# Optimization experiments

Measured on AMD Instinct MI355X. Metric: run time of the kernel, lower is better.

## Reference

```python
import jax, jax.numpy as jnp
import numpy as np
import math

HEADS = 12
D_MODEL = 768
D_K = D_MODEL // HEADS


def setup_inputs() -> dict:
    key = jax.random.key(0)
    ks = jax.random.split(key, 11)
    B, S, D = 2, 2048, D_MODEL
    p = 0.02
    return {
        "query": jax.random.normal(ks[0], (B, S, D), jnp.float32),
        "key": jax.random.normal(ks[1], (B, S, D), jnp.float32),
        "value": jax.random.normal(ks[2], (B, S, D), jnp.float32),
        "Wq": jax.random.normal(ks[3], (D, D), jnp.float32) * p,
        "bq": jax.random.normal(ks[4], (D,), jnp.float32) * p,
        "Wk": jax.random.normal(ks[5], (D, D), jnp.float32) * p,
        "bk": jax.random.normal(ks[6], (D,), jnp.float32) * p,
        "Wv": jax.random.normal(ks[7], (D, D), jnp.float32) * p,
        "bv": jax.random.normal(ks[8], (D,), jnp.float32) * p,
        "Wo": jax.random.normal(ks[9], (D, D), jnp.float32) * p,
        "bo": jax.random.normal(ks[10], (D,), jnp.float32) * p,
    }


def reference(query, key, value, Wq, bq, Wk, bk, Wv, bv, Wo, bo):
    B, S, D = query.shape
    scale = 1.0 / math.sqrt(D_K)
    # Linear projections then split into heads: [B,S,H,Dk]
    q = (query @ Wq + bq).reshape(B, S, HEADS, D_K)
    k = (key @ Wk + bk).reshape(B, S, HEADS, D_K)
    v = (value @ Wv + bv).reshape(B, S, HEADS, D_K)
    # Full score tensor [B, i, j, H]
    scores = jnp.einsum('bihd,bjhd->bijh', q, k) * scale
    # Faithful to source: nn.Softmax(dim=1) over [b,i,j,h] -> query axis i
    attn = jax.nn.softmax(scores, axis=1)
    # dropout_prob=0 (inference/deterministic reference)
    x = jnp.einsum('bijh,bjhd->bihd', attn, v).reshape(B, S, D)
    return x @ Wo + bo
```

## Files before the change

kernel.cpp:

```cpp
#include <hip/hip_runtime.h>
#include <stdint.h>

#define HEADS 12
#define DK 64
#define DM 768
#define BT 2
#define SEQ 2048
#define ROWS (BT*SEQ)

typedef __bf16 bf16x4 __attribute__((ext_vector_type(4)));
typedef __bf16 bf16x8 __attribute__((ext_vector_type(8)));
typedef float f32x4 __attribute__((ext_vector_type(4)));

#define SCL2 0.18033688011112042f

__device__ __forceinline__ float exp2fast(float x) {
#if __has_builtin(__builtin_amdgcn_exp2f)
    return __builtin_amdgcn_exp2f(x);
#else
    return exp2f(x);
#endif
}
__device__ __forceinline__ float log2fast(float x) {
#if __has_builtin(__builtin_amdgcn_logf)
    return __builtin_amdgcn_logf(x);
#else
    return log2f(x);
#endif
}

__device__ __forceinline__ uint16_t f2bf(float f) {
    union { float f; uint32_t u; } v; v.f = f;
    uint32_t u = v.u;
    return (uint16_t)((u + 0x7FFFu + ((u >> 16) & 1u)) >> 16);
}

union U8 { uint16_t u[8]; bf16x8 v; float4 f; };

__device__ __forceinline__ bf16x8 cat44(bf16x4 lo, bf16x4 hi) {
    bf16x8 f;
    f[0] = lo[0]; f[1] = lo[1]; f[2] = lo[2]; f[3] = lo[3];
    f[4] = hi[0]; f[5] = hi[1]; f[6] = hi[2]; f[7] = hi[3];
    return f;
}

__device__ __forceinline__ bf16x8 ldfrag(const char* p) {
    bf16x4 lo = *(const bf16x4*)p;
    bf16x4 hi = *(const bf16x4*)(p + 32);
    return cat44(lo, hi);
}

typedef __attribute__((address_space(3))) void lds_vp;
typedef const __attribute__((address_space(1))) void gbl_vp;
__device__ __forceinline__ void gload16(const void* g, void* l) {
    __builtin_amdgcn_global_load_lds((gbl_vp*)g, (lds_vp*)l, 16, 0, 0);
}

__global__ __launch_bounds__(256) void k_transpose(const float* __restrict__ Wq,
                                                   const float* __restrict__ Wk,
                                                   const float* __restrict__ Wv,
                                                   const float* __restrict__ Wo,
                                                   uint16_t* __restrict__ Wqt,
                                                   uint16_t* __restrict__ Wkt,
                                                   uint16_t* __restrict__ Wvt,
                                                   uint16_t* __restrict__ Wot) {
    __shared__ float t[32][33];
    int z = blockIdx.z;
    const float* W = (z == 0) ? Wq : (z == 1) ? Wk : (z == 2) ? Wv : Wo;
    uint16_t* Wt = (z == 0) ? Wqt : (z == 1) ? Wkt : (z == 2) ? Wvt : Wot;
    int bx = blockIdx.x * 32;
    int by = blockIdx.y * 32;
    int tx = threadIdx.x & 31, ty = threadIdx.x >> 5;
#pragma unroll
    for (int r = 0; r < 32; r += 8)
        t[ty + r][tx] = W[(size_t)(bx + ty + r) * DM + by + tx];
    __syncthreads();
#pragma unroll
    for (int r = 0; r < 32; r += 8)
        Wt[(size_t)(by + ty + r) * DM + bx + tx] = f2bf(t[tx][ty + r]);
}

__global__ __launch_bounds__(256) void k_gemm_qkv(const float* __restrict__ Aq,
                                                  const float* __restrict__ Ak,
                                                  const float* __restrict__ Av,
                                                  const uint16_t* __restrict__ Wt,
                                                  const float* __restrict__ bq,
                                                  const float* __restrict__ bk,
                                                  const float* __restrict__ bv,
                                                  uint16_t* __restrict__ Qm,
                                                  uint16_t* __restrict__ Km,
                                                  uint16_t* __restrict__ VT) {
    __shared__ char smem[2 * 2 * 128 * 80];
    const int z = blockIdx.z;
    const float* A = (z == 0) ? Aq : (z == 1) ? Ak : Av;
    const uint16_t* Bt = Wt + (size_t)z * DM * DM;
    const float* bias = (z == 0) ? bq : (z == 1) ? bk : bv;
    const int tid = threadIdx.x, lane = tid & 63, w = tid >> 6;
    const int q = lane >> 4, r16 = lane & 15;
    const int mtile = blockIdx.y * 128, ntile = blockIdx.x * 128;
    const int wm = (w >> 1) * 64, wn = (w & 1) * 64;
    const int srow = tid >> 1, shalf = tid & 1;
    const float* ap = A + (size_t)(mtile + srow) * DM + shalf * 16;
    const uint16_t* bp = Bt + (size_t)(ntile + srow) * DM + shalf * 16;
    f32x4 acc[4][4] = {};
    float4 ra0 = *(const float4*)(ap + 0);
    float4 ra1 = *(const float4*)(ap + 4);
    float4 ra2 = *(const float4*)(ap + 8);
    float4 ra3 = *(const float4*)(ap + 12);
    float4 rb0 = *(const float4*)bp;
    float4 rb1 = *(const float4*)((const char*)bp + 16);
    for (int t = 0; t < 24; ++t) {
        char* As = smem + (t & 1) * 20480;
        char* Bs = As + 10240;
        U8 pk0, pk1;
        pk0.u[0] = f2bf(ra0.x); pk0.u[1] = f2bf(ra0.y); pk0.u[2] = f2bf(ra0.z); pk0.u[3] = f2bf(ra0.w);
        pk0.u[4] = f2bf(ra1.x); pk0.u[5] = f2bf(ra1.y); pk0.u[6] = f2bf(ra1.z); pk0.u[7] = f2bf(ra1.w);
        pk1.u[0] = f2bf(ra2.x); pk1.u[1] = f2bf(ra2.y); pk1.u[2] = f2bf(ra2.z); pk1.u[3] = f2bf(ra2.w);
        pk1.u[4] = f2bf(ra3.x); pk1.u[5] = f2bf(ra3.y); pk1.u[6] = f2bf(ra3.z); pk1.u[7] = f2bf(ra3.w);
        *(float4*)(As + srow * 80 + shalf * 32) = pk0.f;
        *(float4*)(As + srow * 80 + shalf * 32 + 16) = pk1.f;
        *(float4*)(Bs + srow * 80 + shalf * 32) = rb0;
        *(float4*)(Bs + srow * 80 + shalf * 32 + 16) = rb1;
        if (t < 23) {
            const float* ap2 = ap + (t + 1) * 32;
            ra0 = *(const float4*)(ap2 + 0);
            ra1 = *(const float4*)(ap2 + 4);
            ra2 = *(const float4*)(ap2 + 8);
            ra3 = *(const float4*)(ap2 + 12);
            const uint16_t* bp2 = bp + (t + 1) * 32;
            rb0 = *(const float4*)bp2;
            rb1 = *(const float4*)((const char*)bp2 + 16);
        }
        __syncthreads();
        bf16x8 af[4], bfr[4];
#pragma unroll
        for (int i = 0; i < 4; i++) {
            af[i] = ldfrag(As + (wm + i * 16 + r16) * 80 + q * 8);
            bfr[i] = ldfrag(Bs + (wn + i * 16 + r16) * 80 + q * 8);
        }
#pragma unroll
        for (int mi = 0; mi < 4; mi++)
#pragma unroll
            for (int ni = 0; ni < 4; ni++)
                acc[mi][ni] = __builtin_amdgcn_mfma_f32_16x16x32_bf16(
                    af[mi], bfr[ni], acc[mi][ni], 0, 0, 0);
    }
    if (z < 2) {
        uint16_t* out = (z == 0) ? Qm : Km;
#pragma unroll
        for (int ni = 0; ni < 4; ni++) {
            int n = ntile + wn + ni * 16 + r16;
            float bv2 = bias[n];
#pragma unroll
            for (int mi = 0; mi < 4; mi++)
#pragma unroll
                for (int r = 0; r < 4; r++) {
                    int m = mtile + wm + mi * 16 + 4 * q + r;
                    out[(size_t)m * DM + n] = f2bf(acc[mi][ni][r] + bv2);
                }
        }
    } else {
#pragma unroll
        for (int ni = 0; ni < 4; ni++) {
            int n = ntile + wn + ni * 16 + r16;
            int h = n >> 6, dk = n & 63;
            float bv2 = bias[n];
#pragma unroll
            for (int mi = 0; mi < 4; mi++) {
                int mbase = mtile + wm + mi * 16 + 4 * q;
                int b = mbase >> 11, s = mbase & 2047;
                ushort4 o;
                o.x = f2bf(acc[mi][ni][0] + bv2);
                o.y = f2bf(acc[mi][ni][1] + bv2);
                o.z = f2bf(acc[mi][ni][2] + bv2);
                o.w = f2bf(acc[mi][ni][3] + bv2);
                *(ushort4*)(VT + ((size_t)((b * HEADS + h) * DK + dk)) * SEQ + s) = o;
            }
        }
    }
}

__global__ __launch_bounds__(256) void k_gemm_o(const uint16_t* __restrict__ A,
                                                const uint16_t* __restrict__ Bt,
                                                const float* __restrict__ bias,
                                                float* __restrict__ C) {
    __shared__ char smem[2 * 2 * 128 * 80];
    const int tid = threadIdx.x, lane = tid & 63, w = tid >> 6;
    const int q = lane >> 4, r16 = lane & 15;
    const int mtile = blockIdx.y * 128, ntile = blockIdx.x * 128;
    const int wm = (w >> 1) * 64, wn = (w & 1) * 64;
    const int srow = tid >> 1, shalf = tid & 1;
    const uint16_t* ap = A + (size_t)(mtile + srow) * DM + shalf * 16;
    const uint16_t* bp = Bt + (size_t)(ntile + srow) * DM + shalf * 16;
    f32x4 acc[4][4] = {};
    float4 ra0 = *(const float4*)ap;
    float4 ra1 = *(const float4*)((const char*)ap + 16);
    float4 rb0 = *(const float4*)bp;
    float4 rb1 = *(const float4*)((const char*)bp + 16);
    for (int t = 0; t < 24; ++t) {
        char* As = smem + (t & 1) * 20480;
        char* Bs = As + 10240;
        *(float4*)(As + srow * 80 + shalf * 32) = ra0;
        *(float4*)(As + srow * 80 + shalf * 32 + 16) = ra1;
        *(float4*)(Bs + srow * 80 + shalf * 32) = rb0;
        *(float4*)(Bs + srow * 80 + shalf * 32 + 16) = rb1;
        if (t < 23) {
            const uint16_t* ap2 = ap + (t + 1) * 32;
            ra0 = *(const float4*)ap2;
            ra1 = *(const float4*)((const char*)ap2 + 16);
            const uint16_t* bp2 = bp + (t + 1) * 32;
            rb0 = *(const float4*)bp2;
            rb1 = *(const float4*)((const char*)bp2 + 16);
        }
        __syncthreads();
        bf16x8 af[4], bfr[4];
#pragma unroll
        for (int i = 0; i < 4; i++) {
            af[i] = ldfrag(As + (wm + i * 16 + r16) * 80 + q * 8);
            bfr[i] = ldfrag(Bs + (wn + i * 16 + r16) * 80 + q * 8);
        }
#pragma unroll
        for (int mi = 0; mi < 4; mi++)
#pragma unroll
            for (int ni = 0; ni < 4; ni++)
                acc[mi][ni] = __builtin_amdgcn_mfma_f32_16x16x32_bf16(
                    af[mi], bfr[ni], acc[mi][ni], 0, 0, 0);
    }
#pragma unroll
    for (int ni = 0; ni < 4; ni++) {
        int n = ntile + wn + ni * 16 + r16;
        float bv = bias[n];
#pragma unroll
        for (int mi = 0; mi < 4; mi++)
#pragma unroll
            for (int r = 0; r < 4; r++) {
                int m = mtile + wm + mi * 16 + 4 * q + r;
                C[(size_t)m * DM + n] = acc[mi][ni][r] + bv;
            }
    }
}

__global__ __launch_bounds__(128, 2) void k_stats(const uint16_t* __restrict__ Qm,
                                                  const uint16_t* __restrict__ Km,
                                                  float* __restrict__ L2buf) {
    __shared__ char lds[2 * 8192];
    const int tid = threadIdx.x, lane = tid & 63;
    const int w = tid >> 6;
    const int q = lane >> 4, r16 = lane & 15;
    const int bh = blockIdx.y, b = bh / HEADS, h = bh % HEADS;
    const int j0 = blockIdx.x * 128 + w * 64;
    const uint16_t* Qbase = Qm + (size_t)b * SEQ * DM + h * DK;
    bf16x8 kf[4][2];
#pragma unroll
    for (int jf = 0; jf < 4; jf++) {
        const uint16_t* kp = Km + (size_t)(b * SEQ + j0 + jf * 16 + r16) * DM + h * DK + q * 4;
#pragma unroll
        for (int ks = 0; ks < 2; ks++)
            kf[jf][ks] = cat44(*(const bf16x4*)(kp + ks * 32),
                               *(const bf16x4*)(kp + ks * 32 + 16));
    }
    float Zs[4][4] = {};
#pragma unroll
    for (int c = 0; c < 4; c++) {
        int n = c * 128 + tid, row = n >> 3, u = n & 7;
        gload16(Qbase + (size_t)row * DM + ((u ^ (row & 7)) * 8), lds + n * 16);
    }
    for (int t = 0; t < 32; ++t) {
        asm volatile("s_waitcnt vmcnt(0)" ::: "memory");
        __builtin_amdgcn_s_barrier();
        if (t < 31) {
            char* nb = lds + ((t + 1) & 1) * 8192;
            int i1 = (t + 1) * 64;
#pragma unroll
            for (int c = 0; c < 4; c++) {
                int n = c * 128 + tid, row = n >> 3, u = n & 7;
                gload16(Qbase + (size_t)(i1 + row) * DM + ((u ^ (row & 7)) * 8), nb + n * 16);
            }
        }
        const char* Qs = lds + (t & 1) * 8192;
#pragma unroll
        for (int f = 0; f < 4; f++) {
            bf16x8 qfr[2];
#pragma unroll
            for (int ks = 0; ks < 2; ks++) {
                int row = f * 16 + r16;
                int ulo = (ks * 4 + (q >> 1)) ^ (row & 7);
                int uhi = (ks * 4 + 2 + (q >> 1)) ^ (row & 7);
                qfr[ks] = cat44(*(const bf16x4*)(Qs + row * 128 + ulo * 16 + (q & 1) * 8),
                                *(const bf16x4*)(Qs + row * 128 + uhi * 16 + (q & 1) * 8));
            }
            f32x4 st[4] = {};
#pragma unroll
            for (int jf = 0; jf < 4; jf++)
#pragma unroll
                for (int ks = 0; ks < 2; ks++)
                    st[jf] = __builtin_amdgcn_mfma_f32_16x16x32_bf16(kf[jf][ks], qfr[ks], st[jf], 0, 0, 0);
#pragma unroll
            for (int jf = 0; jf < 4; jf++)
#pragma unroll
                for (int r = 0; r < 4; r++)
                    Zs[jf][r] += exp2fast(st[jf][r] * SCL2);
        }
    }
#pragma unroll
    for (int jf = 0; jf < 4; jf++)
#pragma unroll
        for (int r = 0; r < 4; r++) {
            float e = Zs[jf][r];
#pragma unroll
            for (int m = 1; m < 16; m <<= 1) e += __shfl_xor(e, m);
            if (r16 == 0)
                L2buf[(size_t)bh * SEQ + j0 + jf * 16 + 4 * q + r] = -log2fast(e);
        }
}

__global__ __launch_bounds__(128, 2) void k_attn(const uint16_t* __restrict__ Qm,
                                                 const uint16_t* __restrict__ Km,
                                                 const uint16_t* __restrict__ VT,
                                                 const float* __restrict__ L2,
                                                 uint16_t* __restrict__ Xm) {
    __shared__ char lds[2 * 16384];
    const int tid = threadIdx.x, lane = tid & 63, w = tid >> 6;
    const int q = lane >> 4, r16 = lane & 15;
    const int bh = blockIdx.y, b = bh / HEADS, h = bh % HEADS;
    const int i0 = blockIdx.x * 128 + w * 64;
    const uint16_t* Qbase = Qm + (size_t)b * SEQ * DM + h * DK;
    const uint16_t* Kbase = Km + (size_t)b * SEQ * DM + h * DK;
    const uint16_t* VTb = VT + (size_t)bh * DK * SEQ;
    const float* L2b = L2 + (size_t)bh * SEQ;
    bf16x8 qf[4][2];
#pragma unroll
    for (int ig = 0; ig < 4; ig++) {
        const uint16_t* qp = Qbase + (size_t)(i0 + ig * 16 + r16) * DM + q * 4;
#pragma unroll
        for (int ks = 0; ks < 2; ks++)
            qf[ig][ks] = cat44(*(const bf16x4*)(qp + ks * 32),
                               *(const bf16x4*)(qp + ks * 32 + 16));
    }
    f32x4 xacc[4][4] = {};
#pragma unroll
    for (int c = 0; c < 4; c++) {
        int n = c * 128 + tid, row = n >> 3, u = n & 7;
        gload16(Kbase + (size_t)row * DM + ((u ^ (row & 7)) * 8), lds + n * 16);
        gload16(VTb + (size_t)row * SEQ + ((u ^ (row & 7)) * 8), lds + 8192 + n * 16);
    }
    for (int t = 0; t < 32; ++t) {
        asm volatile("s_waitcnt vmcnt(0)" ::: "memory");
        __builtin_amdgcn_s_barrier();
        if (t < 31) {
            char* nb = lds + ((t + 1) & 1) * 16384;
            int js1 = (t + 1) * 64;
#pragma unroll
            for (int c = 0; c < 4; c++) {
                int n = c * 128 + tid, row = n >> 3, u = n & 7;
                gload16(Kbase + (size_t)(js1 + row) * DM + ((u ^ (row & 7)) * 8), nb + n * 16);
                gload16(VTb + (size_t)row * SEQ + js1 + ((u ^ (row & 7)) * 8), nb + 8192 + n * 16);
            }
        }
        const char* Ks = lds + (t & 1) * 16384;
        const char* Vs = Ks + 8192;
        const int js = t * 64;
        bf16x8 kf[4][2], vf[4][2];
#pragma unroll
        for (int jf = 0; jf < 4; jf++)
#pragma unroll
            for (int ks = 0; ks < 2; ks++) {
                int row = jf * 16 + r16;
                int ulo = (ks * 4 + (q >> 1)) ^ (row & 7);
                int uhi = (ks * 4 + 2 + (q >> 1)) ^ (row & 7);
                kf[jf][ks] = cat44(*(const bf16x4*)(Ks + row * 128 + ulo * 16 + (q & 1) * 8),
                                   *(const bf16x4*)(Ks + row * 128 + uhi * 16 + (q & 1) * 8));
            }
#pragma unroll
        for (int dc = 0; dc < 4; dc++)
#pragma unroll
            for (int c = 0; c < 2; c++) {
                int row = dc * 16 + r16;
                int ulo = (c * 4 + (q >> 1)) ^ (row & 7);
                int uhi = (c * 4 + 2 + (q >> 1)) ^ (row & 7);
                vf[dc][c] = cat44(*(const bf16x4*)(Vs + row * 128 + ulo * 16 + (q & 1) * 8),
                                  *(const bf16x4*)(Vs + row * 128 + uhi * 16 + (q & 1) * 8));
            }
        float l2v[4][4];
#pragma unroll
        for (int jf = 0; jf < 4; jf++) {
            float4 lv = *(const float4*)(L2b + js + jf * 16 + 4 * q);
            l2v[jf][0] = lv.x; l2v[jf][1] = lv.y; l2v[jf][2] = lv.z; l2v[jf][3] = lv.w;
        }
#pragma unroll
        for (int ig = 0; ig < 4; ig++) {
            f32x4 st[4] = {};
#pragma unroll
            for (int jf = 0; jf < 4; jf++)
#pragma unroll
                for (int ks = 0; ks < 2; ks++)
                    st[jf] = __builtin_amdgcn_mfma_f32_16x16x32_bf16(kf[jf][ks], qf[ig][ks], st[jf], 0, 0, 0);
            bf16x8 pb[2];
#pragma unroll
            for (int c = 0; c < 2; c++) {
                U8 t8;
#pragma unroll
                for (int r = 0; r < 4; r++) {
                    t8.u[r]     = f2bf(exp2fast(st[2 * c][r] * SCL2 + l2v[2 * c][r]));
                    t8.u[4 + r] = f2bf(exp2fast(st[2 * c + 1][r] * SCL2 + l2v[2 * c + 1][r]));
                }
                pb[c] = t8.v;
            }
#pragma unroll
            for (int dc = 0; dc < 4; dc++)
#pragma unroll
                for (int c = 0; c < 2; c++)
                    xacc[dc][ig] = __builtin_amdgcn_mfma_f32_16x16x32_bf16(vf[dc][c], pb[c], xacc[dc][ig], 0, 0, 0);
        }
    }
    __syncthreads();
    char* xr = lds + w * 9216;
#pragma unroll
    for (int dc = 0; dc < 4; dc++)
#pragma unroll
        for (int ig = 0; ig < 4; ig++) {
            bf16x4 pk;
            pk[0] = (__bf16)xacc[dc][ig][0];
            pk[1] = (__bf16)xacc[dc][ig][1];
            pk[2] = (__bf16)xacc[dc][ig][2];
            pk[3] = (__bf16)xacc[dc][ig][3];
            *(bf16x4*)(xr + (ig * 16 + r16) * 144 + (dc * 16 + 4 * q) * 2) = pk;
        }
    __syncthreads();
#pragma unroll
    for (int rr = 0; rr < 8; rr++) {
        int row = rr * 8 + (lane >> 3), seg = lane & 7;
        *(float4*)(Xm + (size_t)(b * SEQ + i0 + row) * DM + h * DK + seg * 8) =
            *(const float4*)(xr + row * 144 + seg * 16);
    }
}

extern "C" void kernel_launch(void* const* d_in, const int* in_sizes, int n_in,
                              void* d_out, int out_size, void* d_ws, size_t ws_size,
                              hipStream_t stream) {
    const float* query = (const float*)d_in[0];
    const float* key = (const float*)d_in[1];
    const float* value = (const float*)d_in[2];
    const float* Wq = (const float*)d_in[3];
    const float* bq = (const float*)d_in[4];
    const float* Wk = (const float*)d_in[5];
    const float* bk = (const float*)d_in[6];
    const float* Wv = (const float*)d_in[7];
    const float* bv = (const float*)d_in[8];
    const float* Wo = (const float*)d_in[9];
    const float* bo = (const float*)d_in[10];
    float* out = (float*)d_out;
    char* ws = (char*)d_ws;

    const size_t SZ = (size_t)ROWS * DM * 2;
    const size_t WSZ = (size_t)DM * DM * 2;
    uint16_t* Qm = (uint16_t*)(ws + 0 * SZ);
    uint16_t* Km = (uint16_t*)(ws + 1 * SZ);
    uint16_t* VT = (uint16_t*)(ws + 2 * SZ);
    uint16_t* Xm = (uint16_t*)(ws + 3 * SZ);
    uint16_t* Wqt = (uint16_t*)(ws + 4 * SZ);
    uint16_t* Wkt = (uint16_t*)(ws + 4 * SZ + WSZ);
    uint16_t* Wvt = (uint16_t*)(ws + 4 * SZ + 2 * WSZ);
    uint16_t* Wot = (uint16_t*)(ws + 4 * SZ + 3 * WSZ);
    float* L2buf = (float*)(ws + 4 * SZ + 4 * WSZ);

    k_transpose<<<dim3(24, 24, 4), 256, 0, stream>>>(Wq, Wk, Wv, Wo, Wqt, Wkt, Wvt, Wot);
    k_gemm_qkv<<<dim3(6, 32, 3), 256, 0, stream>>>(query, key, value, Wqt, bq, bk, bv, Qm, Km, VT);
    k_stats<<<dim3(16, 24), 128, 0, stream>>>(Qm, Km, L2buf);
    k_attn<<<dim3(16, 24), 128, 0, stream>>>(Qm, Km, VT, L2buf, Xm);
    k_gemm_o<<<dim3(6, 32), 256, 0, stream>>>(Xm, Wot, bo, out);
}
```

Before: 296.1 us.

## Use 4-wave blocks with 4-deep LDS prefetch pipeline in stats and attention kernels

Both attention-side kernels move from 2 waves per block to 4, with each wave covering 32 rows instead of 64, so the per-wave register footprint shrinks and the same block tile is shared by more waves. The single double-buffered load is replaced by a 4-slot ring that prefetches two tiles ahead, using partial vmcnt waits so loads overlap compute. K and Q fragments are now staged through LDS, and the L2 normalisers are cached in LDS instead of being re-read from global memory. In exchange the kernels use more LDS per block, which may limit how many blocks fit per CU.

```diff
diff --git a/kernel.cpp b/kernel.cpp
--- a/kernel.cpp
+++ b/kernel.cpp
@@ -48,6 +48,13 @@
     bf16x4 lo = *(const bf16x4*)p;
     bf16x4 hi = *(const bf16x4*)(p + 32);
     return cat44(lo, hi);
+}
+
+__device__ __forceinline__ bf16x8 ldswz(const char* base, int row, int ks, int q) {
+    int ulo = (ks * 4 + (q >> 1)) ^ (row & 7);
+    int uhi = (ks * 4 + 2 + (q >> 1)) ^ (row & 7);
+    return cat44(*(const bf16x4*)(base + row * 128 + ulo * 16 + (q & 1) * 8),
+                 *(const bf16x4*)(base + row * 128 + uhi * 16 + (q & 1) * 8));
 }
 
 typedef __attribute__((address_space(3))) void lds_vp;
@@ -240,70 +247,70 @@
     }
 }
 
-__global__ __launch_bounds__(128, 2) void k_stats(const uint16_t* __restrict__ Qm,
+__global__ __launch_bounds__(256, 4) void k_stats(const uint16_t* __restrict__ Qm,
                                                   const uint16_t* __restrict__ Km,
                                                   float* __restrict__ L2buf) {
-    __shared__ char lds[2 * 8192];
-    const int tid = threadIdx.x, lane = tid & 63;
-    const int w = tid >> 6;
+    __shared__ char lds[4 * 8192];
+    const int tid = threadIdx.x, lane = tid & 63, w = tid >> 6;
     const int q = lane >> 4, r16 = lane & 15;
     const int bh = blockIdx.y, b = bh / HEADS, h = bh % HEADS;
-    const int j0 = blockIdx.x * 128 + w * 64;
+    const int j0 = blockIdx.x * 128 + w * 32;
     const uint16_t* Qbase = Qm + (size_t)b * SEQ * DM + h * DK;
-    bf16x8 kf[4][2];
-#pragma unroll
-    for (int jf = 0; jf < 4; jf++) {
-        const uint16_t* kp = Km + (size_t)(b * SEQ + j0 + jf * 16 + r16) * DM + h * DK + q * 4;
+    const uint16_t* Kbase = Km + (size_t)(b * SEQ + blockIdx.x * 128) * DM + h * DK;
+
+#pragma unroll
+    for (int c = 0; c < 4; c++) {
+        int n = c * 256 + tid, row = n >> 3, u = n & 7;
+        gload16(Kbase + (size_t)row * DM + ((u ^ (row & 7)) * 8), lds + n * 16);
+    }
+    asm volatile("s_waitcnt vmcnt(0)" ::: "memory");
+    __syncthreads();
+    bf16x8 kf[2][2];
+#pragma unroll
+    for (int jf = 0; jf < 2; jf++)
 #pragma unroll
         for (int ks = 0; ks < 2; ks++)
-            kf[jf][ks] = cat44(*(const bf16x4*)(kp + ks * 32),
-                               *(const bf16x4*)(kp + ks * 32 + 16));
-    }
-    float Zs[4][4] = {};
-#pragma unroll
-    for (int c = 0; c < 4; c++) {
-        int n = c * 128 + tid, row = n >> 3, u = n & 7;
-        gload16(Qbase + (size_t)row * DM + ((u ^ (row & 7)) * 8), lds + n * 16);
-    }
+            kf[jf][ks] = ldswz(lds, w * 32 + jf * 16 + r16, ks, q);
+    __syncthreads();
+
+    auto stage = [&](int tt) {
+        char* buf = lds + (tt & 3) * 8192;
+        int i1 = (tt & 31) * 64;
+#pragma unroll
+        for (int c = 0; c < 2; c++) {
+            int n = c * 256 + tid, row = n >> 3, u = n & 7;
+            gload16(Qbase + (size_t)(i1 + row) * DM + ((u ^ (row & 7)) * 8), buf + n * 16);
+        }
+    };
+    stage(0); stage(1);
+    float Zs[2][4] = {};
     for (int t = 0; t < 32; ++t) {
-        asm volatile("s_waitcnt vmcnt(0)" ::: "memory");
+        stage((t + 2) & 31);
+        asm volatile("s_waitcnt vmcnt(4)" ::: "memory");
+        __builtin_amdgcn_sched_barrier(0);
         __builtin_amdgcn_s_barrier();
-        if (t < 31) {
-            char* nb = lds + ((t + 1) & 1) * 8192;
-            int i1 = (t + 1) * 64;
-#pragma unroll
-            for (int c = 0; c < 4; c++) {
-                int n = c * 128 + tid, row = n >> 3, u = n & 7;
-                gload16(Qbase + (size_t)(i1 + row) * DM + ((u ^ (row & 7)) * 8), nb + n * 16);
-            }
-        }
-        const char* Qs = lds + (t & 1) * 8192;
+        const char* Qs = lds + (t & 3) * 8192;
 #pragma unroll
         for (int f = 0; f < 4; f++) {
             bf16x8 qfr[2];
 #pragma unroll
-            for (int ks = 0; ks < 2; ks++) {
-                int row = f * 16 + r16;
-                int ulo = (ks * 4 + (q >> 1)) ^ (row & 7);
-                int uhi = (ks * 4 + 2 + (q >> 1)) ^ (row & 7);
-                qfr[ks] = cat44(*(const bf16x4*)(Qs + row * 128 + ulo * 16 + (q & 1) * 8),
-                                *(const bf16x4*)(Qs + row * 128 + uhi * 16 + (q & 1) * 8));
-            }
-            f32x4 st[4] = {};
-#pragma unroll
-            for (int jf = 0; jf < 4; jf++)
+            for (int ks = 0; ks < 2; ks++) qfr[ks] = ldswz(Qs, f * 16 + r16, ks, q);
+            f32x4 st[2] = {};
+#pragma unroll
+            for (int jf = 0; jf < 2; jf++)
 #pragma unroll
                 for (int ks = 0; ks < 2; ks++)
                     st[jf] = __builtin_amdgcn_mfma_f32_16x16x32_bf16(kf[jf][ks], qfr[ks], st[jf], 0, 0, 0);
 #pragma unroll
-            for (int jf = 0; jf < 4; jf++)
+            for (int jf = 0; jf < 2; jf++)
 #pragma unroll
                 for (int r = 0; r < 4; r++)
                     Zs[jf][r] += exp2fast(st[jf][r] * SCL2);
         }
     }
-#pragma unroll
-    for (int jf = 0; jf < 4; jf++)
+    asm volatile("s_waitcnt vmcnt(0)" ::: "memory");
+#pragma unroll
+    for (int jf = 0; jf < 2; jf++)
 #pragma unroll
         for (int r = 0; r < 4; r++) {
             float e = Zs[jf][r];
@@ -314,81 +321,81 @@
         }
 }
 
-__global__ __launch_bounds__(128, 2) void k_attn(const uint16_t* __restrict__ Qm,
+__global__ __launch_bounds__(256, 2) void k_attn(const uint16_t* __restrict__ Qm,
                                                  const uint16_t* __restrict__ Km,
                                                  const uint16_t* __restrict__ VT,
                                                  const float* __restrict__ L2,
                                                  uint16_t* __restrict__ Xm) {
-    __shared__ char lds[2 * 16384];
+    __shared__ char lds[4 * 16384 + 8192];
+    char* L2s = lds + 65536;
     const int tid = threadIdx.x, lane = tid & 63, w = tid >> 6;
     const int q = lane >> 4, r16 = lane & 15;
     const int bh = blockIdx.y, b = bh / HEADS, h = bh % HEADS;
-    const int i0 = blockIdx.x * 128 + w * 64;
-    const uint16_t* Qbase = Qm + (size_t)b * SEQ * DM + h * DK;
+    const int iblk = blockIdx.x * 128;
+    const uint16_t* Qbase = Qm + (size_t)(b * SEQ + iblk) * DM + h * DK;
     const uint16_t* Kbase = Km + (size_t)b * SEQ * DM + h * DK;
     const uint16_t* VTb = VT + (size_t)bh * DK * SEQ;
     const float* L2b = L2 + (size_t)bh * SEQ;
-    bf16x8 qf[4][2];
-#pragma unroll
-    for (int ig = 0; ig < 4; ig++) {
-        const uint16_t* qp = Qbase + (size_t)(i0 + ig * 16 + r16) * DM + q * 4;
+
+    {
+        int o = tid * 32;
+        *(float4*)(L2s + o) = *(const float4*)((const char*)L2b + o);
+        *(float4*)(L2s + o + 16) = *(const float4*)((const char*)L2b + o + 16);
+    }
+#pragma unroll
+    for (int c = 0; c < 4; c++) {
+        int n = c * 256 + tid, row = n >> 3, u = n & 7;
+        gload16(Qbase + (size_t)row * DM + ((u ^ (row & 7)) * 8), lds + n * 16);
+    }
+    asm volatile("s_waitcnt vmcnt(0)" ::: "memory");
+    __syncthreads();
+    bf16x8 qf[2][2];
+#pragma unroll
+    for (int ig = 0; ig < 2; ig++)
 #pragma unroll
         for (int ks = 0; ks < 2; ks++)
-            qf[ig][ks] = cat44(*(const bf16x4*)(qp + ks * 32),
-                               *(const bf16x4*)(qp + ks * 32 + 16));
-    }
-    f32x4 xacc[4][4] = {};
-#pragma unroll
-    for (int c = 0; c < 4; c++) {
-        int n = c * 128 + tid, row = n >> 3, u = n & 7;
-        gload16(Kbase + (size_t)row * DM + ((u ^ (row & 7)) * 8), lds + n * 16);
-        gload16(VTb + (size_t)row * SEQ + ((u ^ (row & 7)) * 8), lds + 8192 + n * 16);
-    }
+            qf[ig][ks] = ldswz(lds, w * 32 + ig * 16 + r16, ks, q);
+    __syncthreads();
+
+    auto stage = [&](int tt) {
+        char* buf = lds + (tt & 3) * 16384;
+        int js1 = (tt & 31) * 64;
+#pragma unroll
+        for (int c = 0; c < 2; c++) {
+            int n = c * 256 + tid, row = n >> 3, u = n & 7;
+            gload16(Kbase + (size_t)(js1 + row) * DM + ((u ^ (row & 7)) * 8), buf + n * 16);
+            gload16(VTb + (size_t)row * SEQ + js1 + ((u ^ (row & 7)) * 8), buf + 8192 + n * 16);
+        }
+    };
+    stage(0); stage(1);
+    f32x4 xacc[4][2] = {};
     for (int t = 0; t < 32; ++t) {
-        asm volatile("s_waitcnt vmcnt(0)" ::: "memory");
+        stage((t + 2) & 31);
+        asm volatile("s_waitcnt vmcnt(8)" ::: "memory");
+        __builtin_amdgcn_sched_barrier(0);
         __builtin_amdgcn_s_barrier();
-        if (t < 31) {
-            char* nb = lds + ((t + 1) & 1) * 16384;
-            int js1 = (t + 1) * 64;
-#pragma unroll
-            for (int c = 0; c < 4; c++) {
-                int n = c * 128 + tid, row = n >> 3, u = n & 7;
-                gload16(Kbase + (size_t)(js1 + row) * DM + ((u ^ (row & 7)) * 8), nb + n * 16);
-                gload16(VTb + (size_t)row * SEQ + js1 + ((u ^ (row & 7)) * 8), nb + 8192 + n * 16);
-            }
-        }
-        const char* Ks = lds + (t & 1) * 16384;
+        const char* Ks = lds + (t & 3) * 16384;
         const char* Vs = Ks + 8192;
         const int js = t * 64;
         bf16x8 kf[4][2], vf[4][2];
 #pragma unroll
         for (int jf = 0; jf < 4; jf++)
 #pragma unroll
-            for (int ks = 0; ks < 2; ks++) {
-                int row = jf * 16 + r16;
-                int ulo = (ks * 4 + (q >> 1)) ^ (row & 7);
-                int uhi = (ks * 4 + 2 + (q >> 1)) ^ (row & 7);
-                kf[jf][ks] = cat44(*(const bf16x4*)(Ks + row * 128 + ulo * 16 + (q & 1) * 8),
-                                   *(const bf16x4*)(Ks + row * 128 + uhi * 16 + (q & 1) * 8));
-            }
+            for (int ks = 0; ks < 2; ks++)
+                kf[jf][ks] = ldswz(Ks, jf * 16 + r16, ks, q);
 #pragma unroll
         for (int dc = 0; dc < 4; dc++)
 #pragma unroll
-            for (int c = 0; c < 2; c++) {
-                int row = dc * 16 + r16;
-                int ulo = (c * 4 + (q >> 1)) ^ (row & 7);
-                int uhi = (c * 4 + 2 + (q >> 1)) ^ (row & 7);
-                vf[dc][c] = cat44(*(const bf16x4*)(Vs + row * 128 + ulo * 16 + (q & 1) * 8),
-                                  *(const bf16x4*)(Vs + row * 128 + uhi * 16 + (q & 1) * 8));
-            }
-        float l2v[4][4];
+            for (int c = 0; c < 2; c++)
+                vf[dc][c] = ldswz(Vs, dc * 16 + r16, c, q);
+        float l2a[4][4];
 #pragma unroll
         for (int jf = 0; jf < 4; jf++) {
-            float4 lv = *(const float4*)(L2b + js + jf * 16 + 4 * q);
-            l2v[jf][0] = lv.x; l2v[jf][1] = lv.y; l2v[jf][2] = lv.z; l2v[jf][3] = lv.w;
-        }
-#pragma unroll
-        for (int ig = 0; ig < 4; ig++) {
+            float4 lv = *(const float4*)(L2s + (js + jf * 16 + 4 * q) * 4);
+            l2a[jf][0] = lv.x; l2a[jf][1] = lv.y; l2a[jf][2] = lv.z; l2a[jf][3] = lv.w;
+        }
+#pragma unroll
+        for (int ig = 0; ig < 2; ig++) {
             f32x4 st[4] = {};
 #pragma unroll
             for (int jf = 0; jf < 4; jf++)
@@ -401,8 +408,8 @@
                 U8 t8;
 #pragma unroll
                 for (int r = 0; r < 4; r++) {
-                    t8.u[r]     = f2bf(exp2fast(st[2 * c][r] * SCL2 + l2v[2 * c][r]));
-                    t8.u[4 + r] = f2bf(exp2fast(st[2 * c + 1][r] * SCL2 + l2v[2 * c + 1][r]));
+                    t8.u[r]     = f2bf(exp2fast(st[2 * c][r] * SCL2 + l2a[2 * c][r]));
+                    t8.u[4 + r] = f2bf(exp2fast(st[2 * c + 1][r] * SCL2 + l2a[2 * c + 1][r]));
                 }
                 pb[c] = t8.v;
             }
@@ -413,12 +420,13 @@
                     xacc[dc][ig] = __builtin_amdgcn_mfma_f32_16x16x32_bf16(vf[dc][c], pb[c], xacc[dc][ig], 0, 0, 0);
         }
     }
-    __syncthreads();
-    char* xr = lds + w * 9216;
+    asm volatile("s_waitcnt vmcnt(0)" ::: "memory");
+    __syncthreads();
+    char* xr = lds + w * 4608;
 #pragma unroll
     for (int dc = 0; dc < 4; dc++)
 #pragma unroll
-        for (int ig = 0; ig < 4; ig++) {
+        for (int ig = 0; ig < 2; ig++) {
             bf16x4 pk;
             pk[0] = (__bf16)xacc[dc][ig][0];
             pk[1] = (__bf16)xacc[dc][ig][1];
@@ -428,9 +436,10 @@
         }
     __syncthreads();
 #pragma unroll
-    for (int rr = 0; rr < 8; rr++) {
-        int row = rr * 8 + (lane >> 3), seg = lane & 7;
-        *(float4*)(Xm + (size_t)(b * SEQ + i0 + row) * DM + h * DK + seg * 8) =
+    for (int cc = 0; cc < 4; cc++) {
+        int uidx = cc * 64 + lane;
+        int row = uidx >> 3, seg = uidx & 7;
+        *(float4*)(Xm + (size_t)(b * SEQ + iblk + w * 32 + row) * DM + h * DK + seg * 8) =
             *(const float4*)(xr + row * 144 + seg * 16);
     }
 }
@@ -466,7 +475,7 @@
 
     k_transpose<<<dim3(24, 24, 4), 256, 0, stream>>>(Wq, Wk, Wv, Wo, Wqt, Wkt, Wvt, Wot);
     k_gemm_qkv<<<dim3(6, 32, 3), 256, 0, stream>>>(query, key, value, Wqt, bq, bk, bv, Qm, Km, VT);
-    k_stats<<<dim3(16, 24), 128, 0, stream>>>(Qm, Km, L2buf);
-    k_attn<<<dim3(16, 24), 128, 0, stream>>>(Qm, Km, VT, L2buf, Xm);
+    k_stats<<<dim3(16, 24), 256, 0, stream>>>(Qm, Km, L2buf);
+    k_attn<<<dim3(16, 24), 256, 0, stream>>>(Qm, Km, VT, L2buf, Xm);
     k_gemm_o<<<dim3(6, 32), 256, 0, stream>>>(Xm, Wot, bo, out);
 }
```

Measured after the change: 256.2 us. 13.5% less time.
